# Performance work log

Measured on AMD Instinct MI355X. Metric: run time of the kernel, lower is better.

The kernel has to match this reference:

```python
import jax, jax.numpy as jnp
import numpy as np

G, NP, F = 128, 1024, 16   # graphs, nodes per graph, node feature dim
K = 16                      # kNN neighbors (includes self, as in PyG knn)
H, L, OUT = 64, 64, 128     # edge-MLP hidden, latent, final output dims


def setup_inputs() -> dict:
    key = jax.random.key(0)
    ks = jax.random.split(key, 5)
    def w(i, shape, fan):
        return jax.random.normal(ks[i], shape, jnp.float32) / np.sqrt(fan)
    return {
        "x": jax.random.normal(ks[0], (G * NP, F), jnp.float32),
        "batch": jnp.repeat(jnp.arange(G, dtype=jnp.int32), NP),  # equal-size graphs
        "W1": w(1, (2 * F, H), 2 * F), "b1": jnp.zeros((H,), jnp.float32),
        "W2": w(2, (H, L), H),         "b2": jnp.zeros((L,), jnp.float32),
        "Wf": w(3, (L, OUT), L),       "bf": jnp.zeros((OUT,), jnp.float32),
    }


def reference(x, batch, W1, b1, W2, b2, Wf, bf):
    # batch = repeat(arange(G), NP) -> equal-size graphs, reshape instead of segment ops
    xg = x.reshape(G, NP, F)
    # dynamic kNN within each graph (squared euclidean, self included like PyG knn)
    sq = jnp.sum(xg * xg, axis=-1)                                   # [G,NP]
    dist = sq[:, :, None] + sq[:, None, :] - 2.0 * jnp.einsum('gif,gjf->gij', xg, xg)
    _, idx = jax.lax.top_k(-dist, K)                                 # [G,NP,K]
    # gather neighbor features x_j
    xj = jnp.take_along_axis(xg[:, None, :, :], idx[..., None], axis=2)  # [G,NP,K,F]
    xi = xg[:, :, None, :]                                           # [G,NP,1,F]
    e = jnp.concatenate([jnp.broadcast_to(xi, xj.shape), xj - xi], axis=-1)  # [G,NP,K,2F]
    # edge MLP [2F -> H -> L], ReLU between, plain last layer
    h = jax.nn.relu(e @ W1 + b1)
    h = h @ W2 + b2                                                  # [G,NP,K,L]
    node = jnp.mean(h, axis=2)                                       # mean aggregation  [G,NP,L]
    g = jnp.mean(node, axis=1)                                       # global_mean_pool  [G,L]
    return g @ Wf + bf                                               # final linear     [G,OUT]
```

## Files before the change

kernel.cpp:

```cpp
#include <hip/hip_runtime.h>
#include <hip/hip_bf16.h>
#include <stdint.h>

#define G_    128
#define NP_   1024
#define F_    16
#define K_    16
#define H_    64
#define L_    64
#define OUT_  128

typedef short  short8v  __attribute__((ext_vector_type(8)));
typedef float  f32x16   __attribute__((ext_vector_type(16)));
typedef float  f32x4    __attribute__((ext_vector_type(4)));

__device__ __forceinline__ uint16_t bf_rne(float f) {
    uint32_t u = __float_as_uint(f);
    return (uint16_t)((u + 0x7FFFu + ((u >> 16) & 1u)) >> 16);
}
__device__ __forceinline__ float bf_to_f(uint16_t h) {
    return __uint_as_float((uint32_t)h << 16);
}

__global__ __launch_bounds__(512, 4) void knn_kernel(
    const float* __restrict__ x, int* __restrict__ idxw)
{
    __shared__ uint16_t zh[2048 * 8];
    __shared__ uint16_t zl[2048 * 8];
    __shared__ float    sqarr[32 * 2 * 16];

    const int b   = blockIdx.x;
    const int g   = b >> 2;
    const float* xg = x + (size_t)g * NP_ * F_;
    const int tid  = threadIdx.x;
    const int lane = tid & 63;
    const int wave = tid >> 6;
    const int hi   = lane >> 5;
    const int col  = lane & 31;

#pragma unroll
    for (int rr = 0; rr < 2; ++rr) {
        const int row = tid * 2 + rr;
        const float4* xr = (const float4*)(xg + (size_t)row * 16);
        float4 c0 = xr[0], c1 = xr[1], c2 = xr[2], c3 = xr[3];
        float fv[16] = {c0.x,c0.y,c0.z,c0.w, c1.x,c1.y,c1.z,c1.w,
                        c2.x,c2.y,c2.z,c2.w, c3.x,c3.y,c3.z,c3.w};
        float sq = 0.f;
#pragma unroll
        for (int e = 0; e < 16; ++e) sq = fmaf(fv[e], fv[e], sq);

        short8v hv0, hv1, lv0, lv1;
#pragma unroll
        for (int e = 0; e < 8; ++e) {
            uint16_t hb = bf_rne(fv[e]);
            hv0[e] = (short)hb;
            lv0[e] = (short)bf_rne(fv[e] - bf_to_f(hb));
        }
#pragma unroll
        for (int e = 0; e < 8; ++e) {
            uint16_t hb = bf_rne(fv[8 + e]);
            hv1[e] = (short)hb;
            lv1[e] = (short)bf_rne(fv[8 + e] - bf_to_f(hb));
        }
        const int e0 = ((row >> 5) << 6) + (row & 31);
        *(short8v*)&zh[(size_t)e0 * 8]        = hv0;
        *(short8v*)&zh[(size_t)(e0 + 32) * 8] = hv1;
        *(short8v*)&zl[(size_t)e0 * 8]        = lv0;
        *(short8v*)&zl[(size_t)(e0 + 32) * 8] = lv1;
        const int s2 = ((row >> 5) << 1) + ((row >> 2) & 1);
        const int r  = (row & 3) | (((row >> 3) & 3) << 2);
        sqarr[s2 * 16 + r] = sq;
    }

    const int qbase = (b & 3) * 256 + wave * 32;
    short8v Bh, Bl;
    {
        const float* qsrc = xg + (size_t)(qbase + col) * 16 + hi * 8;
        float4 q0 = ((const float4*)qsrc)[0];
        float4 q1 = ((const float4*)qsrc)[1];
        float qv[8] = {q0.x,q0.y,q0.z,q0.w, q1.x,q1.y,q1.z,q1.w};
#pragma unroll
        for (int e = 0; e < 8; ++e) {
            float m2 = -2.f * qv[e];
            uint16_t hb = bf_rne(m2);
            Bh[e] = (short)hb;
            Bl[e] = (short)bf_rne(m2 - bf_to_f(hb));
        }
    }

    float hp[16];
#pragma unroll
    for (int m = 0; m < 16; ++m) hp[m] = __uint_as_float(0x7F000000u);

    __syncthreads();

    const int hi4 = hi << 2;
#pragma unroll 4
    for (int s = 0; s < 32; ++s) {
        short8v Ah = *(const short8v*)&zh[(size_t)(s * 64 + lane) * 8];
        short8v Al = *(const short8v*)&zl[(size_t)(s * 64 + lane) * 8];
        const float* sqb = &sqarr[(s * 2 + hi) * 16];
        f32x4 s0 = *(const f32x4*)(sqb + 0);
        f32x4 s1 = *(const f32x4*)(sqb + 4);
        f32x4 s2 = *(const f32x4*)(sqb + 8);
        f32x4 s3 = *(const f32x4*)(sqb + 12);

        f32x16 acc = {0,0,0,0,0,0,0,0,0,0,0,0,0,0,0,0};
        acc = __builtin_amdgcn_mfma_f32_32x32x16_bf16(Ah, Bl, acc, 0, 0, 0);
        acc = __builtin_amdgcn_mfma_f32_32x32x16_bf16(Al, Bh, acc, 0, 0, 0);
        acc = __builtin_amdgcn_mfma_f32_32x32x16_bf16(Ah, Bh, acc, 0, 0, 0);

        const uint32_t orb = ((uint32_t)s << 5) | (uint32_t)hi4;
#define KEY_INS(r, sqv)                                                       \
        {                                                                     \
            float d = acc[r] + (sqv);                                         \
            uint32_t kb = (__float_as_uint(d) & 0xFFFFFC00u) | orb            \
                          | (uint32_t)(((r) & 3) + 8 * ((r) >> 2));           \
            float kf = __uint_as_float(kb);                                   \
            _Pragma("unroll")                                                 \
            for (int m = 15; m >= 1; --m)                                     \
                hp[m] = __builtin_amdgcn_fmed3f(kf, hp[m - 1], hp[m]);        \
            hp[0] = fminf(hp[0], kf);                                         \
        }
        KEY_INS(0,  s0[0]) KEY_INS(1,  s0[1]) KEY_INS(2,  s0[2]) KEY_INS(3,  s0[3])
        KEY_INS(4,  s1[0]) KEY_INS(5,  s1[1]) KEY_INS(6,  s1[2]) KEY_INS(7,  s1[3])
        KEY_INS(8,  s2[0]) KEY_INS(9,  s2[1]) KEY_INS(10, s2[2]) KEY_INS(11, s2[3])
        KEY_INS(12, s3[0]) KEY_INS(13, s3[1]) KEY_INS(14, s3[2]) KEY_INS(15, s3[3])
#undef KEY_INS
    }

    float ot[16];
#pragma unroll
    for (int m = 0; m < 16; ++m) ot[m] = __shfl_xor(hp[m], 32);
#pragma unroll
    for (int m = 0; m < 16; ++m) {
        float kf = ot[m];
#pragma unroll
        for (int t = 15; t >= 1; --t)
            hp[t] = __builtin_amdgcn_fmed3f(kf, hp[t - 1], hp[t]);
        hp[0] = fminf(hp[0], kf);
    }

    if (lane < 32) {
        int* row = idxw + ((size_t)g * NP_ + qbase + col) * K_;
#pragma unroll
        for (int m4 = 0; m4 < 4; ++m4) {
            int4 o;
            o.x = (int)(__float_as_uint(hp[m4 * 4 + 0]) & 1023u);
            o.y = (int)(__float_as_uint(hp[m4 * 4 + 1]) & 1023u);
            o.z = (int)(__float_as_uint(hp[m4 * 4 + 2]) & 1023u);
            o.w = (int)(__float_as_uint(hp[m4 * 4 + 3]) & 1023u);
            *(int4*)(row + m4 * 4) = o;
        }
    }
}

__global__ __launch_bounds__(256) void v_kernel(
    const float* __restrict__ x, const float* __restrict__ W1,
    float* __restrict__ v)
{
    const int lane = threadIdx.x & 63;
    const int wave = threadIdx.x >> 6;

    float wb[16];
#pragma unroll
    for (int f = 0; f < 16; ++f) wb[f] = W1[(16 + f) * 64 + lane];

    const int base = blockIdx.x * 64 + wave * 16;
    for (int n = 0; n < 16; ++n) {
        const int p = base + n;
        const float4* xr = (const float4*)(x + (size_t)p * 16);
        float4 a0 = xr[0], a1 = xr[1], a2 = xr[2], a3 = xr[3];
        float xv[16] = {a0.x,a0.y,a0.z,a0.w, a1.x,a1.y,a1.z,a1.w,
                        a2.x,a2.y,a2.z,a2.w, a3.x,a3.y,a3.z,a3.w};
        float vv = 0.f;
#pragma unroll
        for (int f = 0; f < 16; ++f) vv = fmaf(xv[f], wb[f], vv);
        v[(size_t)p * 64 + lane] = vv;
    }
}

__global__ __launch_bounds__(256) void gather_kernel(
    const float* __restrict__ x, const float* __restrict__ W1,
    const float* __restrict__ b1, const float* __restrict__ v,
    const int* __restrict__ idxw, float* __restrict__ P)
{
    const int lane = threadIdx.x & 63;
    const int wave = threadIdx.x >> 6;
    const int b    = blockIdx.x;
    const int xcd  = b & 7, slot = b >> 3;
    const int g    = xcd + ((slot & 15) << 3);
    const int chunk = slot >> 4;
    const int pbase = g * NP_ + chunk * 128 + wave * 32;

    float wd[16];
#pragma unroll
    for (int f = 0; f < 16; ++f)
        wd[f] = W1[f * 64 + lane] - W1[(16 + f) * 64 + lane];
    const float bias = b1[lane];

    const float* vg = v + ((size_t)g << 16);
    float acc = 0.f;
    for (int n = 0; n < 32; ++n) {
        const int ii = pbase + n;
        const float4* xr = (const float4*)(x + (size_t)ii * 16);
        float4 c0 = xr[0], c1 = xr[1], c2 = xr[2], c3 = xr[3];
        float uu = bias;
        uu = fmaf(c0.x, wd[0],  uu); uu = fmaf(c0.y, wd[1],  uu);
        uu = fmaf(c0.z, wd[2],  uu); uu = fmaf(c0.w, wd[3],  uu);
        uu = fmaf(c1.x, wd[4],  uu); uu = fmaf(c1.y, wd[5],  uu);
        uu = fmaf(c1.z, wd[6],  uu); uu = fmaf(c1.w, wd[7],  uu);
        uu = fmaf(c2.x, wd[8],  uu); uu = fmaf(c2.y, wd[9],  uu);
        uu = fmaf(c2.z, wd[10], uu); uu = fmaf(c2.w, wd[11], uu);
        uu = fmaf(c3.x, wd[12], uu); uu = fmaf(c3.y, wd[13], uu);
        uu = fmaf(c3.z, wd[14], uu); uu = fmaf(c3.w, wd[15], uu);

        const int4* irow = (const int4*)(idxw + (size_t)ii * 16);
#pragma unroll
        for (int q = 0; q < 4; ++q) {
            int4 j4 = irow[q];
            float v0 = vg[((size_t)j4.x << 6) + lane];
            float v1 = vg[((size_t)j4.y << 6) + lane];
            float v2 = vg[((size_t)j4.z << 6) + lane];
            float v3 = vg[((size_t)j4.w << 6) + lane];
            acc += fmaxf(0.f, uu + v0);
            acc += fmaxf(0.f, uu + v1);
            acc += fmaxf(0.f, uu + v2);
            acc += fmaxf(0.f, uu + v3);
        }
    }
    P[(size_t)(((g << 3) + chunk) * 4 + wave) * 64 + lane] = acc;
}

__global__ __launch_bounds__(128) void head_kernel(
    const float* __restrict__ P, const float* __restrict__ W2,
    const float* __restrict__ b2, const float* __restrict__ Wf,
    const float* __restrict__ bf, float* __restrict__ out)
{
    __shared__ float hbar[64];
    __shared__ float t[64];
    const int g = blockIdx.x;
    const int tid = threadIdx.x;
    if (tid < 64) {
        float s = 0.f;
        const float* pr = P + (size_t)g * 32 * 64 + tid;
#pragma unroll
        for (int i = 0; i < 32; ++i) s += pr[i * 64];
        hbar[tid] = s * (1.f / (1024.f * 16.f));
    }
    __syncthreads();
    if (tid < 64) {
        float a = b2[tid];
        for (int h = 0; h < 64; ++h) a = fmaf(hbar[h], W2[h * 64 + tid], a);
        t[tid] = a;
    }
    __syncthreads();
    float a = bf[tid];
    for (int h = 0; h < 64; ++h) a = fmaf(t[h], Wf[h * 128 + tid], a);
    out[g * 128 + tid] = a;
}

extern "C" void kernel_launch(void* const* d_in, const int* in_sizes, int n_in,
                              void* d_out, int out_size, void* d_ws, size_t ws_size,
                              hipStream_t stream)
{
    const float* x  = (const float*)d_in[0];
    const float* W1 = (const float*)d_in[2];
    const float* b1 = (const float*)d_in[3];
    const float* W2 = (const float*)d_in[4];
    const float* b2 = (const float*)d_in[5];
    const float* Wf = (const float*)d_in[6];
    const float* bf = (const float*)d_in[7];
    float* out = (float*)d_out;

    char* ws = (char*)d_ws;
    const size_t MB = 1024 * 1024;
    float* v    = (float*)ws;
    int*   idxw = (int*)(ws + 32 * MB);
    float* P    = (float*)(ws + 40 * MB);

    knn_kernel   <<<G_ * 4, 512, 0, stream>>>(x, idxw);
    v_kernel     <<<2048, 256, 0, stream>>>(x, W1, v);
    gather_kernel<<<G_ * 8, 256, 0, stream>>>(x, W1, b1, v, idxw, P);
    head_kernel  <<<G_, 128, 0, stream>>>(P, W2, b2, Wf, bf, out);
}
```

Before: 163.3 us.

## Replace per-key top-k insertion with sorting network and bitonic merge

Each tile of 16 distance keys is now sorted with a comparator network and merged into the running top-16 using a bitonic half-cleaner, instead of inserting every key with a chain of fmed3. The squared-norm term is also folded into the MFMA accumulator initialisation, removing separate adds. The goal is fewer VALU ops per tile in the selection loop. In exchange, the sort and merge arrays may raise register pressure, and the unroll factor is reduced to compensate.

```diff
diff --git a/kernel.cpp b/kernel.cpp
--- a/kernel.cpp
+++ b/kernel.cpp
@@ -95,39 +95,68 @@
     __syncthreads();
 
     const int hi4 = hi << 2;
-#pragma unroll 4
+
+#define CE(a, i, j) { float t_lo = fminf(a[i], a[j]);                         \
+                      float t_hi = fmaxf(a[i], a[j]);                         \
+                      a[i] = t_lo; a[j] = t_hi; }
+
+#pragma unroll 2
     for (int s = 0; s < 32; ++s) {
         short8v Ah = *(const short8v*)&zh[(size_t)(s * 64 + lane) * 8];
         short8v Al = *(const short8v*)&zl[(size_t)(s * 64 + lane) * 8];
         const float* sqb = &sqarr[(s * 2 + hi) * 16];
-        f32x4 s0 = *(const f32x4*)(sqb + 0);
-        f32x4 s1 = *(const f32x4*)(sqb + 4);
-        f32x4 s2 = *(const f32x4*)(sqb + 8);
-        f32x4 s3 = *(const f32x4*)(sqb + 12);
-
-        f32x16 acc = {0,0,0,0,0,0,0,0,0,0,0,0,0,0,0,0};
+        f32x4 q0 = *(const f32x4*)(sqb + 0);
+        f32x4 q1 = *(const f32x4*)(sqb + 4);
+        f32x4 q2 = *(const f32x4*)(sqb + 8);
+        f32x4 q3 = *(const f32x4*)(sqb + 12);
+
+        f32x16 acc = {q0[0],q0[1],q0[2],q0[3], q1[0],q1[1],q1[2],q1[3],
+                      q2[0],q2[1],q2[2],q2[3], q3[0],q3[1],q3[2],q3[3]};
         acc = __builtin_amdgcn_mfma_f32_32x32x16_bf16(Ah, Bl, acc, 0, 0, 0);
         acc = __builtin_amdgcn_mfma_f32_32x32x16_bf16(Al, Bh, acc, 0, 0, 0);
         acc = __builtin_amdgcn_mfma_f32_32x32x16_bf16(Ah, Bh, acc, 0, 0, 0);
 
-        const uint32_t orb = ((uint32_t)s << 5) | (uint32_t)hi4;
-#define KEY_INS(r, sqv)                                                       \
-        {                                                                     \
-            float d = acc[r] + (sqv);                                         \
-            uint32_t kb = (__float_as_uint(d) & 0xFFFFFC00u) | orb            \
-                          | (uint32_t)(((r) & 3) + 8 * ((r) >> 2));           \
-            float kf = __uint_as_float(kb);                                   \
-            _Pragma("unroll")                                                 \
-            for (int m = 15; m >= 1; --m)                                     \
-                hp[m] = __builtin_amdgcn_fmed3f(kf, hp[m - 1], hp[m]);        \
-            hp[0] = fminf(hp[0], kf);                                         \
-        }
-        KEY_INS(0,  s0[0]) KEY_INS(1,  s0[1]) KEY_INS(2,  s0[2]) KEY_INS(3,  s0[3])
-        KEY_INS(4,  s1[0]) KEY_INS(5,  s1[1]) KEY_INS(6,  s1[2]) KEY_INS(7,  s1[3])
-        KEY_INS(8,  s2[0]) KEY_INS(9,  s2[1]) KEY_INS(10, s2[2]) KEY_INS(11, s2[3])
-        KEY_INS(12, s3[0]) KEY_INS(13, s3[1]) KEY_INS(14, s3[2]) KEY_INS(15, s3[3])
-#undef KEY_INS
-    }
+        const uint32_t jb = ((uint32_t)s << 5) | (uint32_t)hi4;
+        float kk[16];
+#pragma unroll
+        for (int r = 0; r < 16; ++r) {
+            uint32_t jv = jb | (uint32_t)((r & 3) + 8 * (r >> 2));
+            kk[r] = __uint_as_float((__float_as_uint(acc[r]) & 0xFFFFFC00u) | jv);
+        }
+
+        CE(kk,0,1)  CE(kk,2,3)  CE(kk,4,5)  CE(kk,6,7)
+        CE(kk,8,9)  CE(kk,10,11) CE(kk,12,13) CE(kk,14,15)
+        CE(kk,0,2)  CE(kk,1,3)  CE(kk,4,6)  CE(kk,5,7)
+        CE(kk,8,10) CE(kk,9,11) CE(kk,12,14) CE(kk,13,15)
+        CE(kk,1,2)  CE(kk,5,6)  CE(kk,9,10) CE(kk,13,14)
+        CE(kk,0,4)  CE(kk,1,5)  CE(kk,2,6)  CE(kk,3,7)
+        CE(kk,8,12) CE(kk,9,13) CE(kk,10,14) CE(kk,11,15)
+        CE(kk,2,4)  CE(kk,3,5)  CE(kk,10,12) CE(kk,11,13)
+        CE(kk,1,2)  CE(kk,3,4)  CE(kk,5,6)
+        CE(kk,9,10) CE(kk,11,12) CE(kk,13,14)
+        CE(kk,0,8)  CE(kk,1,9)  CE(kk,2,10) CE(kk,3,11)
+        CE(kk,4,12) CE(kk,5,13) CE(kk,6,14) CE(kk,7,15)
+        CE(kk,4,8)  CE(kk,5,9)  CE(kk,6,10) CE(kk,7,11)
+        CE(kk,2,4)  CE(kk,3,5)  CE(kk,6,8)  CE(kk,7,9)
+        CE(kk,10,12) CE(kk,11,13)
+        CE(kk,1,2)  CE(kk,3,4)  CE(kk,5,6)  CE(kk,7,8)
+        CE(kk,9,10) CE(kk,11,12) CE(kk,13,14)
+
+        float c[16];
+#pragma unroll
+        for (int i = 0; i < 16; ++i) c[i] = fminf(hp[i], kk[15 - i]);
+        CE(c,0,8)  CE(c,1,9)  CE(c,2,10) CE(c,3,11)
+        CE(c,4,12) CE(c,5,13) CE(c,6,14) CE(c,7,15)
+        CE(c,0,4)  CE(c,1,5)  CE(c,2,6)  CE(c,3,7)
+        CE(c,8,12) CE(c,9,13) CE(c,10,14) CE(c,11,15)
+        CE(c,0,2)  CE(c,1,3)  CE(c,4,6)  CE(c,5,7)
+        CE(c,8,10) CE(c,9,11) CE(c,12,14) CE(c,13,15)
+        CE(c,0,1)  CE(c,2,3)  CE(c,4,5)  CE(c,6,7)
+        CE(c,8,9)  CE(c,10,11) CE(c,12,13) CE(c,14,15)
+#pragma unroll
+        for (int i = 0; i < 16; ++i) hp[i] = c[i];
+    }
+#undef CE
 
     float ot[16];
 #pragma unroll
```

After: 148.5 us. 1.1x faster.
